# Performance work log

Measured on AMD Instinct MI355X. Metric: run time of the kernel, lower is better.

## Reference

```python
import jax, jax.numpy as jnp
import numpy as np

ALPHA = 1.0
TAKT = 700


def _overlap_penalty(perm, sizes, takt):
    # perm: [B,T] int predicted station per sequence slot; sizes: [B,V] int (V==T)
    B, T = perm.shape
    sz = jnp.take_along_axis(sizes, perm, axis=1)  # [B,T] job size at each slot

    # Offset recurrence: only the immediately previous allocation at the SAME
    # station contributes (the prev_seq==seq_num branch in the torch code is
    # unreachable since allocations are appended after processing).
    def step(carry, inp):
        prev_perm, prev_end = carry  # prev_end = size + offset of previous slot
        p, s = inp
        o = jnp.where(p == prev_perm, jnp.maximum(prev_end - takt, 0), 0)
        return (p, s + o), o

    init = (jnp.full((B,), -1, perm.dtype), jnp.zeros((B,), sz.dtype))
    _, offs = jax.lax.scan(step, init, (perm.T, sz.T))  # offs: [T,B]
    offs = offs.T  # [B,T]

    xs = jnp.arange(T, dtype=offs.dtype)[None, :] * takt + offs  # [B,T] start
    xe = xs + sz  # [B,T] end

    # Count pairs (t, t') with t' < t, same station, overlapping intervals.
    prior = jnp.tril(jnp.ones((T, T), dtype=bool), k=-1)  # [t, t'] : t' < t
    same = perm[:, :, None] == perm[:, None, :]
    ov = (xs[:, :, None] < xe[:, None, :]) & (xe[:, :, None] > xs[:, None, :])
    count = jnp.sum(same & ov & prior[None, :, :])
    return count.astype(jnp.float32) / B


def reference(logits, tgt, sizes):
    # logits: [B,T,V], tgt: [B,T] int, sizes: [B,V] int
    logp = jax.nn.log_softmax(logits, axis=-1)
    ce = -jnp.mean(jnp.take_along_axis(logp, tgt[..., None].astype(jnp.int32), axis=-1))
    pred = jnp.argmax(logits, axis=-1).astype(jnp.int32)  # [B,T]
    ov = _overlap_penalty(pred, sizes, TAKT)
    return ce + ALPHA * ov


def setup_inputs() -> dict:
    key = jax.random.key(0)
    k1, k2, k3 = jax.random.split(key, 3)
    B, T, V = 32, 1024, 1024
    logits = jax.random.normal(k1, (B, T, V), dtype=jnp.float32)
    tgt = jax.random.randint(k2, (B, T), 0, V, dtype=jnp.int32)
    sizes = jax.random.randint(k3, (B, V), 0, 1400, dtype=jnp.int32)
    return {"logits": logits, "tgt": tgt, "sizes": sizes}
```

## Files before the change

### kernel.cpp

```cpp
#include <hip/hip_runtime.h>

#define TAKT 700
#define B 32
#define T 1024
#define V 1024

__global__ __launch_bounds__(256) void row_kernel(const float* __restrict__ logits,
                                                  const int* __restrict__ tgt,
                                                  float* __restrict__ rowloss,
                                                  int* __restrict__ pred) {
    const int wave = threadIdx.x >> 6;
    const int lane = threadIdx.x & 63;
    const int row  = blockIdx.x * 4 + wave;

    const float4* base = reinterpret_cast<const float4*>(logits + (size_t)row * V);
    float4 v[4];
#pragma unroll
    for (int k = 0; k < 4; ++k) v[k] = base[lane + 64 * k];

    float m = v[0].x; int mi = lane * 4;
#pragma unroll
    for (int k = 0; k < 4; ++k) {
        const float* q = reinterpret_cast<const float*>(&v[k]);
#pragma unroll
        for (int j = 0; j < 4; ++j) {
            const float x = q[j];
            const int idx = lane * 4 + k * 256 + j;
            if (x > m) { m = x; mi = idx; }
        }
    }

#pragma unroll
    for (int off = 32; off > 0; off >>= 1) {
        const float om = __shfl_xor(m, off, 64);
        const int   oi = __shfl_xor(mi, off, 64);
        if (om > m || (om == m && oi < mi)) { m = om; mi = oi; }
    }

    float s = 0.f;
#pragma unroll
    for (int k = 0; k < 4; ++k) {
        const float* q = reinterpret_cast<const float*>(&v[k]);
#pragma unroll
        for (int j = 0; j < 4; ++j) s += __expf(q[j] - m);
    }
#pragma unroll
    for (int off = 32; off > 0; off >>= 1) s += __shfl_xor(s, off, 64);

    const int tg = tgt[row];
    const int q4 = tg >> 2;
    const int srcLane = q4 & 63;
    const int kk = q4 >> 6;
    const int jj = tg & 3;
    const float4 vk = (kk == 0) ? v[0] : (kk == 1) ? v[1] : (kk == 2) ? v[2] : v[3];
    const float xl = (jj == 0) ? vk.x : (jj == 1) ? vk.y : (jj == 2) ? vk.z : vk.w;
    const float xt = __shfl(xl, srcLane, 64);

    if (lane == 0) {
        rowloss[row] = logf(s) + m - xt;
        pred[row]    = mi;
    }
}

__global__ __launch_bounds__(256) void overlap_kernel(const int* __restrict__ pred,
                                                      const int* __restrict__ sizes,
                                                      int* __restrict__ counts) {
    const int b     = blockIdx.x >> 4;
    const int chunk = blockIdx.x & 15;
    const int tid   = threadIdx.x;

    __shared__ int  perm_s[T];
    __shared__ int  sz_s[T];
    __shared__ int2 iv_s[T];

    const int* prow = pred  + b * T;
    const int* srow = sizes + b * V;

    for (int t = tid; t < T; t += 256) {
        const int p = prow[t];
        perm_s[t] = p;
        sz_s[t]   = srow[p];
    }
    __syncthreads();

    for (int t = tid; t < T; t += 256) {
        const int p = perm_s[t];
        int acc = 0, o = 0;
        for (int j = t - 1; j >= 0 && perm_s[j] == p; --j) {
            acc += sz_s[j] - TAKT;
            if (acc > o) o = acc;
        }
        const int xs = t * TAKT + o;
        iv_s[t] = make_int2(xs, xs + sz_s[t]);
    }
    __syncthreads();

    const int t   = chunk * 64 + (tid & 63);
    const int sub = tid >> 6;
    const int p = perm_s[t];
    const int2 me = iv_s[t];
    int cnt = 0;
    for (int tp = sub; tp < t; tp += 4) {
        const int2 iv = iv_s[tp];
        cnt += (int)((perm_s[tp] == p) & (me.x < iv.y) & (me.y > iv.x));
    }

    __shared__ int scnt[256];
    scnt[tid] = cnt;
    __syncthreads();
    for (int off = 128; off > 0; off >>= 1) {
        if (tid < off) scnt[tid] += scnt[tid + off];
        __syncthreads();
    }
    if (tid == 0) counts[blockIdx.x] = scnt[0];
}

__global__ __launch_bounds__(256) void final_kernel(const float* __restrict__ rowloss,
                                                    const int* __restrict__ counts,
                                                    float* __restrict__ out) {
    const int tid = threadIdx.x;
    double acc = 0.0;
    const float4* rl4 = reinterpret_cast<const float4*>(rowloss);
    for (int i = tid; i < (B * T) / 4; i += 256) {
        const float4 r = rl4[i];
        acc += (double)r.x + (double)r.y + (double)r.z + (double)r.w;
    }

    __shared__ double sacc[256];
    __shared__ int    scnt[256];
    sacc[tid] = acc;
    scnt[tid] = counts[tid] + counts[tid + 256];
    __syncthreads();
    for (int off = 128; off > 0; off >>= 1) {
        if (tid < off) { sacc[tid] += sacc[tid + off]; scnt[tid] += scnt[tid + off]; }
        __syncthreads();
    }
    if (tid == 0) {
        out[0] = (float)(sacc[0] / (double)(B * T)) + (float)scnt[0] / (float)B;
    }
}

extern "C" void kernel_launch(void* const* d_in, const int* in_sizes, int n_in,
                              void* d_out, int out_size, void* d_ws, size_t ws_size,
                              hipStream_t stream) {
    const float* logits = (const float*)d_in[0];
    const int*   tgt    = (const int*)d_in[1];
    const int*   sizes  = (const int*)d_in[2];
    float* out = (float*)d_out;

    float* rowloss = (float*)d_ws;
    int*   pred    = (int*)((char*)d_ws + (size_t)B * T * 4);
    int*   counts  = (int*)((char*)d_ws + (size_t)B * T * 8);

    row_kernel<<<(B * T) / 4, 256, 0, stream>>>(logits, tgt, rowloss, pred);
    overlap_kernel<<<B * 16, 256, 0, stream>>>(pred, sizes, counts);
    final_kernel<<<1, 256, 0, stream>>>(rowloss, counts, out);
}
```

Measured before the change: 73.21 us.

## Process two rows per wave, restructure argmax, and split overlap work finer

The row kernel now handles two rows per wave. It replaces the sequential compare-and-track argmax with a max pass followed by a fused exp-sum and min-index pass, which raises memory-level parallelism and cuts dependent branches. The overlap kernel splits each batch into 32 chunks of 32 slots with 8 sub-strides instead of 16 chunks of 64. This gives more blocks and better load balance over the triangular pair loop, but each block must recompute the per-batch offsets. Register pressure in the row kernel roughly doubles.

```diff
diff --git a/kernel.cpp b/kernel.cpp
--- a/kernel.cpp
+++ b/kernel.cpp
@@ -4,6 +4,7 @@
 #define B 32
 #define T 1024
 #define V 1024
+#define BIGIDX 0x7fffffff
 
 __global__ __launch_bounds__(256) void row_kernel(const float* __restrict__ logits,
                                                   const int* __restrict__ tgt,
@@ -11,62 +12,74 @@
                                                   int* __restrict__ pred) {
     const int wave = threadIdx.x >> 6;
     const int lane = threadIdx.x & 63;
-    const int row  = blockIdx.x * 4 + wave;
+    const int row0 = blockIdx.x * 8 + wave * 2;
+    const int row1 = row0 + 1;
 
-    const float4* base = reinterpret_cast<const float4*>(logits + (size_t)row * V);
-    float4 v[4];
+    const float4* b0 = reinterpret_cast<const float4*>(logits + (size_t)row0 * V);
+    const float4* b1 = reinterpret_cast<const float4*>(logits + (size_t)row1 * V);
+    float4 v0[4], v1[4];
 #pragma unroll
-    for (int k = 0; k < 4; ++k) v[k] = base[lane + 64 * k];
+    for (int k = 0; k < 4; ++k) { v0[k] = b0[lane + 64 * k]; v1[k] = b1[lane + 64 * k]; }
 
-    float m = v[0].x; int mi = lane * 4;
+    float m0 = v0[0].x, m1 = v1[0].x;
 #pragma unroll
     for (int k = 0; k < 4; ++k) {
-        const float* q = reinterpret_cast<const float*>(&v[k]);
+        const float* q0 = reinterpret_cast<const float*>(&v0[k]);
+        const float* q1 = reinterpret_cast<const float*>(&v1[k]);
+#pragma unroll
+        for (int j = 0; j < 4; ++j) { m0 = fmaxf(m0, q0[j]); m1 = fmaxf(m1, q1[j]); }
+    }
+#pragma unroll
+    for (int off = 32; off > 0; off >>= 1) {
+        m0 = fmaxf(m0, __shfl_xor(m0, off, 64));
+        m1 = fmaxf(m1, __shfl_xor(m1, off, 64));
+    }
+
+    float s0 = 0.f, s1 = 0.f;
+    int i0 = BIGIDX, i1 = BIGIDX;
+#pragma unroll
+    for (int k = 0; k < 4; ++k) {
+        const float* q0 = reinterpret_cast<const float*>(&v0[k]);
+        const float* q1 = reinterpret_cast<const float*>(&v1[k]);
 #pragma unroll
         for (int j = 0; j < 4; ++j) {
-            const float x = q[j];
             const int idx = lane * 4 + k * 256 + j;
-            if (x > m) { m = x; mi = idx; }
+            s0 += __expf(q0[j] - m0);
+            s1 += __expf(q1[j] - m1);
+            i0 = min(i0, (q0[j] == m0) ? idx : BIGIDX);
+            i1 = min(i1, (q1[j] == m1) ? idx : BIGIDX);
         }
     }
-
 #pragma unroll
     for (int off = 32; off > 0; off >>= 1) {
-        const float om = __shfl_xor(m, off, 64);
-        const int   oi = __shfl_xor(mi, off, 64);
-        if (om > m || (om == m && oi < mi)) { m = om; mi = oi; }
+        s0 += __shfl_xor(s0, off, 64);
+        s1 += __shfl_xor(s1, off, 64);
+        i0 = min(i0, __shfl_xor(i0, off, 64));
+        i1 = min(i1, __shfl_xor(i1, off, 64));
     }
 
-    float s = 0.f;
-#pragma unroll
-    for (int k = 0; k < 4; ++k) {
-        const float* q = reinterpret_cast<const float*>(&v[k]);
-#pragma unroll
-        for (int j = 0; j < 4; ++j) s += __expf(q[j] - m);
+    const int tg0 = tgt[row0], tg1 = tgt[row1];
+    {
+        const int q4 = tg0 >> 2, kk = q4 >> 6, jj = tg0 & 3;
+        const float4 vk = (kk == 0) ? v0[0] : (kk == 1) ? v0[1] : (kk == 2) ? v0[2] : v0[3];
+        const float xl = (jj == 0) ? vk.x : (jj == 1) ? vk.y : (jj == 2) ? vk.z : vk.w;
+        const float xt = __shfl(xl, q4 & 63, 64);
+        if (lane == 0) { rowloss[row0] = logf(s0) + m0 - xt; pred[row0] = i0; }
     }
-#pragma unroll
-    for (int off = 32; off > 0; off >>= 1) s += __shfl_xor(s, off, 64);
-
-    const int tg = tgt[row];
-    const int q4 = tg >> 2;
-    const int srcLane = q4 & 63;
-    const int kk = q4 >> 6;
-    const int jj = tg & 3;
-    const float4 vk = (kk == 0) ? v[0] : (kk == 1) ? v[1] : (kk == 2) ? v[2] : v[3];
-    const float xl = (jj == 0) ? vk.x : (jj == 1) ? vk.y : (jj == 2) ? vk.z : vk.w;
-    const float xt = __shfl(xl, srcLane, 64);
-
-    if (lane == 0) {
-        rowloss[row] = logf(s) + m - xt;
-        pred[row]    = mi;
+    {
+        const int q4 = tg1 >> 2, kk = q4 >> 6, jj = tg1 & 3;
+        const float4 vk = (kk == 0) ? v1[0] : (kk == 1) ? v1[1] : (kk == 2) ? v1[2] : v1[3];
+        const float xl = (jj == 0) ? vk.x : (jj == 1) ? vk.y : (jj == 2) ? vk.z : vk.w;
+        const float xt = __shfl(xl, q4 & 63, 64);
+        if (lane == 0) { rowloss[row1] = logf(s1) + m1 - xt; pred[row1] = i1; }
     }
 }
 
 __global__ __launch_bounds__(256) void overlap_kernel(const int* __restrict__ pred,
                                                       const int* __restrict__ sizes,
                                                       int* __restrict__ counts) {
-    const int b     = blockIdx.x >> 4;
-    const int chunk = blockIdx.x & 15;
+    const int b     = blockIdx.x >> 5;
+    const int chunk = blockIdx.x & 31;
     const int tid   = threadIdx.x;
 
     __shared__ int  perm_s[T];
@@ -95,12 +108,12 @@
     }
     __syncthreads();
 
-    const int t   = chunk * 64 + (tid & 63);
-    const int sub = tid >> 6;
+    const int t   = chunk * 32 + (tid & 31);
+    const int sub = tid >> 5;
     const int p = perm_s[t];
     const int2 me = iv_s[t];
     int cnt = 0;
-    for (int tp = sub; tp < t; tp += 4) {
+    for (int tp = sub; tp < t; tp += 8) {
         const int2 iv = iv_s[tp];
         cnt += (int)((perm_s[tp] == p) & (me.x < iv.y) & (me.y > iv.x));
     }
@@ -129,7 +142,7 @@
     __shared__ double sacc[256];
     __shared__ int    scnt[256];
     sacc[tid] = acc;
-    scnt[tid] = counts[tid] + counts[tid + 256];
+    scnt[tid] = counts[tid] + counts[tid + 256] + counts[tid + 512] + counts[tid + 768];
     __syncthreads();
     for (int off = 128; off > 0; off >>= 1) {
         if (tid < off) { sacc[tid] += sacc[tid + off]; scnt[tid] += scnt[tid + off]; }
@@ -152,7 +165,7 @@
     int*   pred    = (int*)((char*)d_ws + (size_t)B * T * 4);
     int*   counts  = (int*)((char*)d_ws + (size_t)B * T * 8);
 
-    row_kernel<<<(B * T) / 4, 256, 0, stream>>>(logits, tgt, rowloss, pred);
-    overlap_kernel<<<B * 16, 256, 0, stream>>>(pred, sizes, counts);
+    row_kernel<<<(B * T) / 8, 256, 0, stream>>>(logits, tgt, rowloss, pred);
+    overlap_kernel<<<B * 32, 256, 0, stream>>>(pred, sizes, counts);
     final_kernel<<<1, 256, 0, stream>>>(rowloss, counts, out);
 }
```

Measured after the change: 72.40 us. No clear change (-1.1%).
